# Kernel tuning notes

Hardware: AMD Instinct MI355X
Metric: run time of the kernel (lower is better)

## Reference

```python
import jax, jax.numpy as jnp
import numpy as np

N = 50000      # num vertices
E = 600000     # num incidence pairs
M = 100000     # num hyperedges
IN = 256       # in_channels
H = 8          # heads
C = 32         # out_channels per head


def setup_inputs() -> dict:
    key = jax.random.key(0)
    k = jax.random.split(key, 5)
    X = jax.random.normal(k[0], (N, IN), jnp.float32)
    W = jax.random.normal(k[1], (IN, H * C), jnp.float32) * (1.0 / np.sqrt(IN))
    att_e = jax.random.normal(k[2], (1, H, C), jnp.float32) * 0.1
    vertex = jax.random.randint(k[3], (E,), 0, N)
    edges = jax.random.randint(k[4], (E,), 0, M)
    return {"X": X, "W": W, "att_e": att_e, "vertex": vertex, "edges": edges, "num_edges": M}


def reference(X, W, att_e, vertex, edges, num_edges):
    n, h, c = X.shape[0], att_e.shape[1], att_e.shape[2]
    X0 = X @ W                              # [N, H*C]
    Xh = X0.reshape(n, h, c)                # [N, H, C]
    Xve = Xh[vertex]                        # [E, H, C] gather node feats per incidence
    # mean-aggregate incidences -> hyperedge features
    cnt = jax.ops.segment_sum(jnp.ones((vertex.shape[0],), X.dtype), edges, num_segments=num_edges)
    Xe = jax.ops.segment_sum(Xve, edges, num_segments=num_edges) / jnp.maximum(cnt, 1.0)[:, None, None]  # [M, H, C]
    alpha_e = jnp.sum(Xe * att_e, axis=-1)  # [M, H]
    a_ev = alpha_e[edges]                   # [E, H]
    alpha = jnp.where(a_ev >= 0, a_ev, 0.2 * a_ev)  # leaky_relu(0.2)
    # numerically stable segment softmax over incidences grouped by vertex
    amax = jax.ops.segment_max(alpha, vertex, num_segments=n)[vertex]
    aexp = jnp.exp(alpha - amax)
    asum = jax.ops.segment_sum(aexp, vertex, num_segments=n)[vertex]
    attn = aexp / (asum + 1e-16)            # [E, H]
    Xev = Xe[edges] * attn[:, :, None]      # [E, H, C]
    Xv = jax.ops.segment_sum(Xev, vertex, num_segments=n)  # [N, H, C]
    return jax.nn.gelu(Xv.reshape(n, h * c), approximate=False)
```

## Files before the change

kernel.cpp:

```cpp
#include <hip/hip_runtime.h>
#include <hip/hip_bf16.h>
#include <math.h>

#define NV 50000
#define NE 600000
#define NM 100000
#define KIN 256
#define HCC 256
#define NHH 8

#define NCH 32
#define CHUNK 18750
#define KRANGE 25000
#define HIST_B (NCH * 6)
#define CSCAN_B 74

#define SCAN_NB0 25
#define SCAN_NB1 13

#define CNT_B 2344
#define GEMM_RG 784
#define GEMM_B (GEMM_RG * 4)

typedef unsigned int u32;
typedef unsigned short u16;
typedef _Float16 f16;
typedef _Float16 v8h __attribute__((ext_vector_type(8)));
typedef _Float16 v4h __attribute__((ext_vector_type(4)));
typedef float v4f __attribute__((ext_vector_type(4)));

__global__ __launch_bounds__(256) void k_hist(const int* __restrict__ vertex,
                                              const int* __restrict__ edges,
                                              u16* __restrict__ r_e,
                                              u16* __restrict__ r_v,
                                              u16* __restrict__ Ce,
                                              u16* __restrict__ Cv) {
    __shared__ __align__(16) u32 hist[KRANGE / 2];
    const int bid = blockIdx.x;
    const int t = threadIdx.x;
    const int pass = bid >> 5;
    const int chunk = bid & (NCH - 1);
    const bool eside = pass < 4;
    const int kbase = (eside ? pass : pass - 4) * KRANGE;
    const int* keys = eside ? edges : vertex;
    u16* rout = eside ? r_e : r_v;
    u16* crow = eside ? (Ce + (size_t)chunk * NM) : (Cv + (size_t)chunk * NV);

    uint4* h4 = (uint4*)hist;
    for (int j = t; j < KRANGE / 8; j += 256) h4[j] = make_uint4(0u, 0u, 0u, 0u);
    __syncthreads();

    const int i0 = chunk * CHUNK;
    for (int i = i0 + t; i < i0 + CHUNK; i += 256) {
        int k = keys[i] - kbase;
        if ((u32)k < (u32)KRANGE) {
            int sh = (k & 1) << 4;
            u32 old = atomicAdd(&hist[k >> 1], 1u << sh);
            rout[i] = (u16)(old >> sh);
        }
    }
    __syncthreads();

    uint4* d4 = (uint4*)(crow + kbase);
    for (int j = t; j < KRANGE / 8; j += 256) d4[j] = h4[j];
}

__global__ __launch_bounds__(1024) void k_cscan(u16* __restrict__ Ce,
                                                u16* __restrict__ Cv,
                                                int* __restrict__ e_start,
                                                int* __restrict__ v_start) {
    int tid = blockIdx.x * 1024 + threadIdx.x;
    u32* mat;
    int* outp;
    int col, ncol;
    if (tid < NM / 2)               { mat = (u32*)Ce; outp = e_start; col = tid;          ncol = NM / 2; }
    else if (tid < NM / 2 + NV / 2) { mat = (u32*)Cv; outp = v_start; col = tid - NM / 2; ncol = NV / 2; }
    else return;
    u32 s = 0;
    u32* p = mat + col;
    for (int c = 0; c < NCH; ++c) {
        u32 o = *p;
        *p = s;
        s += o;
        p += ncol;
    }
    outp[2 * col + 1] = (int)(s & 0xffffu);
    outp[2 * col + 2] = (int)(s >> 16);
}

__global__ __launch_bounds__(256) void k_gemm(const float* __restrict__ X,
                                              const float* __restrict__ W,
                                              f16* __restrict__ X0) {
    __shared__ __align__(16) f16 sA[64][72];
    __shared__ __align__(16) f16 sB[64][72];
    const int g = blockIdx.x;
    const int rg = (g >> 5) * 8 + (g & 7);
    const int cg = (g >> 3) & 3;
    if (rg >= (NV + 63) / 64) return;
    const int t = threadIdx.x;
    const int r0 = rg * 64;
    const int c0 = cg * 64;
    const int wave = t >> 6;
    const int lane = t & 63;
    const int quad = lane >> 4;
    const int l16 = lane & 15;
    const int wr = wave & 1;
    const int wc = wave >> 1;

    v4f acc[2][2] = {{{0.f,0.f,0.f,0.f},{0.f,0.f,0.f,0.f}},
                     {{0.f,0.f,0.f,0.f},{0.f,0.f,0.f,0.f}}};

    for (int kc = 0; kc < KIN; kc += 64) {
        __syncthreads();
        #pragma unroll
        for (int i = 0; i < 4; ++i) {
            int lin = i * 256 + t;
            int row = lin >> 4;
            int k = (lin & 15) * 4;
            int gr = r0 + row;
            float4 x = make_float4(0.f, 0.f, 0.f, 0.f);
            if (gr < NV) x = *(const float4*)(X + (size_t)gr * KIN + kc + k);
            v4h hv = { (f16)x.x, (f16)x.y, (f16)x.z, (f16)x.w };
            *(v4h*)&sA[row][k] = hv;
        }
        #pragma unroll
        for (int i = 0; i < 4; ++i) {
            int lin = i * 256 + t;
            int k = lin >> 4;
            int n = (lin & 15) * 4;
            float4 b = *(const float4*)(W + (size_t)(kc + k) * HCC + c0 + n);
            sB[n + 0][k] = (f16)b.x;
            sB[n + 1][k] = (f16)b.y;
            sB[n + 2][k] = (f16)b.z;
            sB[n + 3][k] = (f16)b.w;
        }
        __syncthreads();
        #pragma unroll
        for (int ks = 0; ks < 2; ++ks) {
            const int kb = ks * 32 + quad * 8;
            v8h a[2], b[2];
            #pragma unroll
            for (int rf = 0; rf < 2; ++rf)
                a[rf] = *(const v8h*)&sA[wr * 32 + rf * 16 + l16][kb];
            #pragma unroll
            for (int cf = 0; cf < 2; ++cf)
                b[cf] = *(const v8h*)&sB[wc * 32 + cf * 16 + l16][kb];
            #pragma unroll
            for (int rf = 0; rf < 2; ++rf)
                #pragma unroll
                for (int cf = 0; cf < 2; ++cf)
                    acc[rf][cf] = __builtin_amdgcn_mfma_f32_16x16x32_f16(a[rf], b[cf], acc[rf][cf], 0, 0, 0);
        }
    }
    #pragma unroll
    for (int rf = 0; rf < 2; ++rf)
        #pragma unroll
        for (int cf = 0; cf < 2; ++cf)
            #pragma unroll
            for (int r = 0; r < 4; ++r) {
                int grow = r0 + wr * 32 + rf * 16 + quad * 4 + r;
                if (grow < NV)
                    X0[(size_t)grow * HCC + c0 + wc * 32 + cf * 16 + l16] = (f16)acc[rf][cf][r];
            }
}

__global__ __launch_bounds__(1024) void k_scan_blk(int* __restrict__ a0,
                                                   int* __restrict__ a1,
                                                   int* __restrict__ bsum) {
    const int b = blockIdx.x;
    int* a;
    int n, base;
    if (b < SCAN_NB0) { a = a0; n = NM + 1; base = b * 4096; }
    else              { a = a1; n = NV + 1; base = (b - SCAN_NB0) * 4096; }
    const int t = threadIdx.x;
    const int lane = t & 63, w = t >> 6;
    const int i = base + t * 4;
    int4 v = make_int4(0, 0, 0, 0);
    if (i + 3 < n) v = *(const int4*)(a + i);
    else if (i < n) {
        v.x = a[i];
        if (i + 1 < n) v.y = a[i + 1];
        if (i + 2 < n) v.z = a[i + 2];
    }
    v.y += v.x; v.z += v.y; v.w += v.z;
    int s = v.w;
    #pragma unroll
    for (int d = 1; d < 64; d <<= 1) {
        int x = __shfl_up(s, d, 64);
        if (lane >= d) s += x;
    }
    __shared__ int partials[16];
    __shared__ int woff[16];
    if (lane == 63) partials[w] = s;
    __syncthreads();
    if (t < 16) {
        int p = partials[t];
        int ps = p;
        #pragma unroll
        for (int d = 1; d < 16; d <<= 1) {
            int x = __shfl_up(ps, d, 64);
            if (t >= d) ps += x;
        }
        woff[t] = ps - p;
        if (t == 15) bsum[b] = ps;
    }
    __syncthreads();
    const int add = (s - v.w) + woff[w];
    v.x += add; v.y += add; v.z += add; v.w += add;
    if (i + 3 < n) *(int4*)(a + i) = v;
    else if (i < n) {
        a[i] = v.x;
        if (i + 1 < n) a[i + 1] = v.y;
        if (i + 2 < n) a[i + 2] = v.z;
    }
}

__global__ __launch_bounds__(1024) void k_scan_add(int* __restrict__ a0,
                                                   int* __restrict__ a1,
                                                   const int* __restrict__ bsum) {
    const int b = blockIdx.x;
    int* a;
    int n, bs0, blocal;
    if (b < SCAN_NB0) { a = a0; n = NM + 1; bs0 = 0;        blocal = b; }
    else              { a = a1; n = NV + 1; bs0 = SCAN_NB0; blocal = b - SCAN_NB0; }
    const int t = threadIdx.x;
    const int lane = t & 63;
    int x = (lane < blocal) ? bsum[bs0 + lane] : 0;
    #pragma unroll
    for (int d = 1; d < 64; d <<= 1) x += __shfl_xor(x, d, 64);
    const int off = x;
    const int i = blocal * 4096 + t * 4;
    if (i + 3 < n) {
        int4 v = *(const int4*)(a + i);
        v.x += off; v.y += off; v.z += off; v.w += off;
        *(int4*)(a + i) = v;
    } else if (i < n) {
        a[i] += off;
        if (i + 1 < n) a[i + 1] += off;
        if (i + 2 < n) a[i + 2] += off;
    }
}

__global__ __launch_bounds__(256) void k_efill(const int* __restrict__ vertex,
                                               const int* __restrict__ edges,
                                               const u16* __restrict__ r_e,
                                               const int* __restrict__ e_start,
                                               const u16* __restrict__ Ce,
                                               int* __restrict__ e_list) {
    int i = blockIdx.x * 256 + threadIdx.x;
    if (i >= NE) return;
    int m = edges[i];
    int chunk = i / CHUNK;
    int pos = e_start[m] + (int)Ce[(size_t)chunk * NM + m] + (int)r_e[i];
    e_list[pos] = vertex[i];
}

__global__ __launch_bounds__(256) void k_vfill_egather(const int* __restrict__ vertex,
                                                       const int* __restrict__ edges,
                                                       const u16* __restrict__ r_v,
                                                       const int* __restrict__ v_start,
                                                       const u16* __restrict__ Cv,
                                                       int* __restrict__ v_list,
                                                       const int* __restrict__ e_start,
                                                       const int* __restrict__ e_list,
                                                       const f16* __restrict__ X0,
                                                       const float* __restrict__ att,
                                                       f16* __restrict__ Xe,
                                                       float* __restrict__ alpha_e) {
    const int bid = blockIdx.x;
    if (bid < CNT_B) {
        int i = bid * 256 + threadIdx.x;
        if (i < NE) {
            int v = vertex[i];
            int chunk = i / CHUNK;
            int pos = v_start[v] + (int)Cv[(size_t)chunk * NV + v] + (int)r_v[i];
            v_list[pos] = edges[i];
        }
        return;
    }
    int m = (bid - CNT_B) * 4 + (threadIdx.x >> 6);
    int lane = threadIdx.x & 63;
    int s0 = e_start[m], s1 = e_start[m + 1];
    int c = lane * 4;
    float4 acc = make_float4(0.f, 0.f, 0.f, 0.f);
    int i = s0;
    for (; i + 3 < s1; i += 4) {
        int v0 = e_list[i], v1 = e_list[i + 1], v2 = e_list[i + 2], v3 = e_list[i + 3];
        v4h x0 = *(const v4h*)(X0 + (size_t)v0 * HCC + c);
        v4h x1 = *(const v4h*)(X0 + (size_t)v1 * HCC + c);
        v4h x2 = *(const v4h*)(X0 + (size_t)v2 * HCC + c);
        v4h x3 = *(const v4h*)(X0 + (size_t)v3 * HCC + c);
        acc.x += (float)x0[0] + (float)x1[0] + (float)x2[0] + (float)x3[0];
        acc.y += (float)x0[1] + (float)x1[1] + (float)x2[1] + (float)x3[1];
        acc.z += (float)x0[2] + (float)x1[2] + (float)x2[2] + (float)x3[2];
        acc.w += (float)x0[3] + (float)x1[3] + (float)x2[3] + (float)x3[3];
    }
    for (; i < s1; ++i) {
        int v0 = e_list[i];
        v4h x0 = *(const v4h*)(X0 + (size_t)v0 * HCC + c);
        acc.x += (float)x0[0];
        acc.y += (float)x0[1];
        acc.z += (float)x0[2];
        acc.w += (float)x0[3];
    }
    float inv = 1.0f / fmaxf((float)(s1 - s0), 1.0f);
    acc.x *= inv; acc.y *= inv; acc.z *= inv; acc.w *= inv;
    v4h xev = { (f16)acc.x, (f16)acc.y, (f16)acc.z, (f16)acc.w };
    *(v4h*)(Xe + (size_t)m * HCC + c) = xev;
    float4 av = *(const float4*)(att + c);
    float p = acc.x * av.x + acc.y * av.y + acc.z * av.z + acc.w * av.w;
    p += __shfl_xor(p, 1, 64);
    p += __shfl_xor(p, 2, 64);
    p += __shfl_xor(p, 4, 64);
    if ((lane & 7) == 0) alpha_e[m * NHH + (lane >> 3)] = p;
}

__global__ __launch_bounds__(256) void k_vertex_gather(const int* __restrict__ v_start,
                                                       const int* __restrict__ v_list,
                                                       const f16* __restrict__ Xe,
                                                       const float* __restrict__ alpha_e,
                                                       float* __restrict__ out) {
    int v = blockIdx.x * 4 + (threadIdx.x >> 6);
    int lane = threadIdx.x & 63;
    int s0 = v_start[v], s1 = v_start[v + 1];
    int h = lane >> 3;
    int c = lane * 4;
    float4 acc = make_float4(0.f, 0.f, 0.f, 0.f);
    float se = 0.f;
    int i = s0;
    for (; i + 1 < s1; i += 2) {
        int m0 = v_list[i], m1 = v_list[i + 1];
        float a0 = alpha_e[m0 * NHH + h];
        float a1 = alpha_e[m1 * NHH + h];
        v4h x0 = *(const v4h*)(Xe + (size_t)m0 * HCC + c);
        v4h x1 = *(const v4h*)(Xe + (size_t)m1 * HCC + c);
        a0 = (a0 >= 0.f) ? a0 : 0.2f * a0;
        a1 = (a1 >= 0.f) ? a1 : 0.2f * a1;
        float e0 = __expf(a0);
        float e1 = __expf(a1);
        acc.x += e0 * (float)x0[0] + e1 * (float)x1[0];
        acc.y += e0 * (float)x0[1] + e1 * (float)x1[1];
        acc.z += e0 * (float)x0[2] + e1 * (float)x1[2];
        acc.w += e0 * (float)x0[3] + e1 * (float)x1[3];
        se += e0 + e1;
    }
    if (i < s1) {
        int m0 = v_list[i];
        float a0 = alpha_e[m0 * NHH + h];
        v4h x0 = *(const v4h*)(Xe + (size_t)m0 * HCC + c);
        a0 = (a0 >= 0.f) ? a0 : 0.2f * a0;
        float e0 = __expf(a0);
        acc.x += e0 * (float)x0[0];
        acc.y += e0 * (float)x0[1];
        acc.z += e0 * (float)x0[2];
        acc.w += e0 * (float)x0[3];
        se += e0;
    }
    float inv = 1.0f / (se + 1e-16f);
    float4 o;
    float xx;
    xx = acc.x * inv; o.x = 0.5f * xx * (1.f + erff(xx * 0.70710678118f));
    xx = acc.y * inv; o.y = 0.5f * xx * (1.f + erff(xx * 0.70710678118f));
    xx = acc.z * inv; o.z = 0.5f * xx * (1.f + erff(xx * 0.70710678118f));
    xx = acc.w * inv; o.w = 0.5f * xx * (1.f + erff(xx * 0.70710678118f));
    *(float4*)(out + (size_t)v * HCC + c) = o;
}

extern "C" void kernel_launch(void* const* d_in, const int* in_sizes, int n_in,
                              void* d_out, int out_size, void* d_ws, size_t ws_size,
                              hipStream_t stream) {
    const float* X = (const float*)d_in[0];
    const float* W = (const float*)d_in[1];
    const float* att = (const float*)d_in[2];
    const int* vertex = (const int*)d_in[3];
    const int* edges = (const int*)d_in[4];
    float* out = (float*)d_out;

    char* ws = (char*)d_ws;
    size_t off = 0;
    #define WS_TAKE(bytes) (ws + off); off += (((size_t)(bytes)) + 15) & ~(size_t)15
    f16* X0 = (f16*)WS_TAKE((size_t)NV * HCC * 2);
    f16* Xe = (f16*)WS_TAKE((size_t)NM * HCC * 2);
    float* alpha_e = (float*)WS_TAKE((size_t)NM * NHH * 4);
    size_t z0 = off;
    int* e_start = (int*)WS_TAKE((size_t)(NM + 1) * 4);
    int* v_start = (int*)WS_TAKE((size_t)(NV + 1) * 4);
    size_t z1 = off;
    int* e_list = (int*)WS_TAKE((size_t)NE * 4);
    int* v_list = (int*)WS_TAKE((size_t)NE * 4);
    u16* r_e = (u16*)WS_TAKE((size_t)NE * 2);
    u16* r_v = (u16*)WS_TAKE((size_t)NE * 2);
    u16* Ce = (u16*)WS_TAKE((size_t)NCH * NM * 2);
    u16* Cv = (u16*)WS_TAKE((size_t)NCH * NV * 2);
    int* bsum = (int*)WS_TAKE(64 * 4);
    #undef WS_TAKE

    hipMemsetAsync(e_start, 0, z1 - z0, stream);

    k_hist<<<HIST_B, 256, 0, stream>>>(vertex, edges, r_e, r_v, Ce, Cv);
    k_cscan<<<CSCAN_B, 1024, 0, stream>>>(Ce, Cv, e_start, v_start);
    k_scan_blk<<<SCAN_NB0 + SCAN_NB1, 1024, 0, stream>>>(e_start, v_start, bsum);
    k_scan_add<<<SCAN_NB0 + SCAN_NB1, 1024, 0, stream>>>(e_start, v_start, bsum);
    k_gemm<<<GEMM_B, 256, 0, stream>>>(X, W, X0);
    k_efill<<<CNT_B, 256, 0, stream>>>(vertex, edges, r_e, e_start, Ce, e_list);
    k_vfill_egather<<<CNT_B + NM / 4, 256, 0, stream>>>(vertex, edges, r_v, v_start, Cv, v_list,
                                                        e_start, e_list, X0, att, Xe, alpha_e);
    k_vertex_gather<<<NV / 4, 256, 0, stream>>>(v_start, v_list, Xe, alpha_e, out);
}
```

Baseline: 328.0 us.

## Fuse histogram with GEMM, merge fill kernels, widen gathers to 8-element halves

Histogram and GEMM blocks now run in one launch, with smem shared between the two roles, so the matmul can overlap the counting pass. The histogram chunk count triples to spread the per-key counting over more blocks. The e-list and v-list fills merge into one kernel, and the hyperedge gather becomes its own launch. Both gather kernels now load 8 halves per lane and split incidences across two half-waves, combined with a cross-half shuffle. In exchange, the count matrices and the column scan grow threefold, and every fused-kernel block reserves the large histogram smem, which may limit GEMM occupancy.

Result: no change. 329.5 us (+0.5%).

```diff
diff --git a/kernel.cpp b/kernel.cpp
--- a/kernel.cpp
+++ b/kernel.cpp
@@ -9,10 +9,11 @@
 #define HCC 256
 #define NHH 8
 
-#define NCH 32
-#define CHUNK 18750
+#define NCH 96
+#define CHUNK 6250
 #define KRANGE 25000
-#define HIST_B (NCH * 6)
+#define NPASS 6
+#define HIST_B (NCH * NPASS)
 #define CSCAN_B 74
 
 #define SCAN_NB0 25
@@ -28,41 +29,120 @@
 typedef _Float16 v8h __attribute__((ext_vector_type(8)));
 typedef _Float16 v4h __attribute__((ext_vector_type(4)));
 typedef float v4f __attribute__((ext_vector_type(4)));
-
-__global__ __launch_bounds__(256) void k_hist(const int* __restrict__ vertex,
-                                              const int* __restrict__ edges,
-                                              u16* __restrict__ r_e,
-                                              u16* __restrict__ r_v,
-                                              u16* __restrict__ Ce,
-                                              u16* __restrict__ Cv) {
-    __shared__ __align__(16) u32 hist[KRANGE / 2];
+typedef float v8f __attribute__((ext_vector_type(8)));
+
+__global__ __launch_bounds__(256) void k_hist_gemm(const int* __restrict__ vertex,
+                                                   const int* __restrict__ edges,
+                                                   u16* __restrict__ r_e,
+                                                   u16* __restrict__ r_v,
+                                                   u16* __restrict__ Ce,
+                                                   u16* __restrict__ Cv,
+                                                   const float* __restrict__ X,
+                                                   const float* __restrict__ W,
+                                                   f16* __restrict__ X0) {
+    __shared__ __align__(16) u32 smem[KRANGE / 2];
     const int bid = blockIdx.x;
     const int t = threadIdx.x;
-    const int pass = bid >> 5;
-    const int chunk = bid & (NCH - 1);
-    const bool eside = pass < 4;
-    const int kbase = (eside ? pass : pass - 4) * KRANGE;
-    const int* keys = eside ? edges : vertex;
-    u16* rout = eside ? r_e : r_v;
-    u16* crow = eside ? (Ce + (size_t)chunk * NM) : (Cv + (size_t)chunk * NV);
-
-    uint4* h4 = (uint4*)hist;
-    for (int j = t; j < KRANGE / 8; j += 256) h4[j] = make_uint4(0u, 0u, 0u, 0u);
-    __syncthreads();
-
-    const int i0 = chunk * CHUNK;
-    for (int i = i0 + t; i < i0 + CHUNK; i += 256) {
-        int k = keys[i] - kbase;
-        if ((u32)k < (u32)KRANGE) {
-            int sh = (k & 1) << 4;
-            u32 old = atomicAdd(&hist[k >> 1], 1u << sh);
-            rout[i] = (u16)(old >> sh);
+    if (bid < HIST_B) {
+        u32* hist = smem;
+        const int pass = bid / NCH;
+        const int chunk = bid % NCH;
+        const bool eside = pass < 4;
+        const int kbase = (eside ? pass : pass - 4) * KRANGE;
+        const int* keys = eside ? edges : vertex;
+        u16* rout = eside ? r_e : r_v;
+        u16* crow = eside ? (Ce + (size_t)chunk * NM) : (Cv + (size_t)chunk * NV);
+
+        uint4* h4 = (uint4*)hist;
+        for (int j = t; j < KRANGE / 8; j += 256) h4[j] = make_uint4(0u, 0u, 0u, 0u);
+        __syncthreads();
+
+        const int i0 = chunk * CHUNK;
+        for (int i = i0 + t; i < i0 + CHUNK; i += 256) {
+            int k = keys[i] - kbase;
+            if ((u32)k < (u32)KRANGE) {
+                int sh = (k & 1) << 4;
+                u32 old = atomicAdd(&hist[k >> 1], 1u << sh);
+                rout[i] = (u16)(old >> sh);
+            }
         }
-    }
-    __syncthreads();
-
-    uint4* d4 = (uint4*)(crow + kbase);
-    for (int j = t; j < KRANGE / 8; j += 256) d4[j] = h4[j];
+        __syncthreads();
+
+        uint4* d4 = (uint4*)(crow + kbase);
+        for (int j = t; j < KRANGE / 8; j += 256) d4[j] = h4[j];
+        return;
+    }
+    typedef f16 (*tile_t)[72];
+    tile_t sA = (tile_t)smem;
+    tile_t sB = (tile_t)((char*)smem + 64 * 72 * 2);
+    const int g = bid - HIST_B;
+    const int rg = (g >> 5) * 8 + (g & 7);
+    const int cg = (g >> 3) & 3;
+    if (rg >= (NV + 63) / 64) return;
+    const int r0 = rg * 64;
+    const int c0 = cg * 64;
+    const int wave = t >> 6;
+    const int lane = t & 63;
+    const int quad = lane >> 4;
+    const int l16 = lane & 15;
+    const int wr = wave & 1;
+    const int wc = wave >> 1;
+
+    v4f acc[2][2] = {{{0.f,0.f,0.f,0.f},{0.f,0.f,0.f,0.f}},
+                     {{0.f,0.f,0.f,0.f},{0.f,0.f,0.f,0.f}}};
+
+    for (int kc = 0; kc < KIN; kc += 64) {
+        __syncthreads();
+        #pragma unroll
+        for (int i = 0; i < 4; ++i) {
+            int lin = i * 256 + t;
+            int row = lin >> 4;
+            int k = (lin & 15) * 4;
+            int gr = r0 + row;
+            float4 x = make_float4(0.f, 0.f, 0.f, 0.f);
+            if (gr < NV) x = *(const float4*)(X + (size_t)gr * KIN + kc + k);
+            v4h hv = { (f16)x.x, (f16)x.y, (f16)x.z, (f16)x.w };
+            *(v4h*)&sA[row][k] = hv;
+        }
+        #pragma unroll
+        for (int i = 0; i < 4; ++i) {
+            int lin = i * 256 + t;
+            int k = lin >> 4;
+            int n = (lin & 15) * 4;
+            float4 b = *(const float4*)(W + (size_t)(kc + k) * HCC + c0 + n);
+            sB[n + 0][k] = (f16)b.x;
+            sB[n + 1][k] = (f16)b.y;
+            sB[n + 2][k] = (f16)b.z;
+            sB[n + 3][k] = (f16)b.w;
+        }
+        __syncthreads();
+        #pragma unroll
+        for (int ks = 0; ks < 2; ++ks) {
+            const int kb = ks * 32 + quad * 8;
+            v8h a[2], b[2];
+            #pragma unroll
+            for (int rf = 0; rf < 2; ++rf)
+                a[rf] = *(const v8h*)&sA[wr * 32 + rf * 16 + l16][kb];
+            #pragma unroll
+            for (int cf = 0; cf < 2; ++cf)
+                b[cf] = *(const v8h*)&sB[wc * 32 + cf * 16 + l16][kb];
+            #pragma unroll
+            for (int rf = 0; rf < 2; ++rf)
+                #pragma unroll
+                for (int cf = 0; cf < 2; ++cf)
+                    acc[rf][cf] = __builtin_amdgcn_mfma_f32_16x16x32_f16(a[rf], b[cf], acc[rf][cf], 0, 0, 0);
+        }
+    }
+    #pragma unroll
+    for (int rf = 0; rf < 2; ++rf)
+        #pragma unroll
+        for (int cf = 0; cf < 2; ++cf)
+            #pragma unroll
+            for (int r = 0; r < 4; ++r) {
+                int grow = r0 + wr * 32 + rf * 16 + quad * 4 + r;
+                if (grow < NV)
+                    X0[(size_t)grow * HCC + c0 + wc * 32 + cf * 16 + l16] = (f16)acc[rf][cf][r];
+            }
 }
 
 __global__ __launch_bounds__(1024) void k_cscan(u16* __restrict__ Ce,
@@ -88,82 +168,6 @@
     outp[2 * col + 2] = (int)(s >> 16);
 }
 
-__global__ __launch_bounds__(256) void k_gemm(const float* __restrict__ X,
-                                              const float* __restrict__ W,
-                                              f16* __restrict__ X0) {
-    __shared__ __align__(16) f16 sA[64][72];
-    __shared__ __align__(16) f16 sB[64][72];
-    const int g = blockIdx.x;
-    const int rg = (g >> 5) * 8 + (g & 7);
-    const int cg = (g >> 3) & 3;
-    if (rg >= (NV + 63) / 64) return;
-    const int t = threadIdx.x;
-    const int r0 = rg * 64;
-    const int c0 = cg * 64;
-    const int wave = t >> 6;
-    const int lane = t & 63;
-    const int quad = lane >> 4;
-    const int l16 = lane & 15;
-    const int wr = wave & 1;
-    const int wc = wave >> 1;
-
-    v4f acc[2][2] = {{{0.f,0.f,0.f,0.f},{0.f,0.f,0.f,0.f}},
-                     {{0.f,0.f,0.f,0.f},{0.f,0.f,0.f,0.f}}};
-
-    for (int kc = 0; kc < KIN; kc += 64) {
-        __syncthreads();
-        #pragma unroll
-        for (int i = 0; i < 4; ++i) {
-            int lin = i * 256 + t;
-            int row = lin >> 4;
-            int k = (lin & 15) * 4;
-            int gr = r0 + row;
-            float4 x = make_float4(0.f, 0.f, 0.f, 0.f);
-            if (gr < NV) x = *(const float4*)(X + (size_t)gr * KIN + kc + k);
-            v4h hv = { (f16)x.x, (f16)x.y, (f16)x.z, (f16)x.w };
-            *(v4h*)&sA[row][k] = hv;
-        }
-        #pragma unroll
-        for (int i = 0; i < 4; ++i) {
-            int lin = i * 256 + t;
-            int k = lin >> 4;
-            int n = (lin & 15) * 4;
-            float4 b = *(const float4*)(W + (size_t)(kc + k) * HCC + c0 + n);
-            sB[n + 0][k] = (f16)b.x;
-            sB[n + 1][k] = (f16)b.y;
-            sB[n + 2][k] = (f16)b.z;
-            sB[n + 3][k] = (f16)b.w;
-        }
-        __syncthreads();
-        #pragma unroll
-        for (int ks = 0; ks < 2; ++ks) {
-            const int kb = ks * 32 + quad * 8;
-            v8h a[2], b[2];
-            #pragma unroll
-            for (int rf = 0; rf < 2; ++rf)
-                a[rf] = *(const v8h*)&sA[wr * 32 + rf * 16 + l16][kb];
-            #pragma unroll
-            for (int cf = 0; cf < 2; ++cf)
-                b[cf] = *(const v8h*)&sB[wc * 32 + cf * 16 + l16][kb];
-            #pragma unroll
-            for (int rf = 0; rf < 2; ++rf)
-                #pragma unroll
-                for (int cf = 0; cf < 2; ++cf)
-                    acc[rf][cf] = __builtin_amdgcn_mfma_f32_16x16x32_f16(a[rf], b[cf], acc[rf][cf], 0, 0, 0);
-        }
-    }
-    #pragma unroll
-    for (int rf = 0; rf < 2; ++rf)
-        #pragma unroll
-        for (int cf = 0; cf < 2; ++cf)
-            #pragma unroll
-            for (int r = 0; r < 4; ++r) {
-                int grow = r0 + wr * 32 + rf * 16 + quad * 4 + r;
-                if (grow < NV)
-                    X0[(size_t)grow * HCC + c0 + wc * 32 + cf * 16 + l16] = (f16)acc[rf][cf][r];
-            }
-}
-
 __global__ __launch_bounds__(1024) void k_scan_blk(int* __restrict__ a0,
                                                    int* __restrict__ a1,
                                                    int* __restrict__ bsum) {
@@ -241,129 +245,129 @@
     }
 }
 
-__global__ __launch_bounds__(256) void k_efill(const int* __restrict__ vertex,
+__global__ __launch_bounds__(256) void k_fill2(const int* __restrict__ vertex,
                                                const int* __restrict__ edges,
                                                const u16* __restrict__ r_e,
+                                               const u16* __restrict__ r_v,
                                                const int* __restrict__ e_start,
+                                               const int* __restrict__ v_start,
                                                const u16* __restrict__ Ce,
-                                               int* __restrict__ e_list) {
+                                               const u16* __restrict__ Cv,
+                                               int* __restrict__ e_list,
+                                               int* __restrict__ v_list) {
     int i = blockIdx.x * 256 + threadIdx.x;
     if (i >= NE) return;
-    int m = edges[i];
+    int v = vertex[i], m = edges[i];
     int chunk = i / CHUNK;
-    int pos = e_start[m] + (int)Ce[(size_t)chunk * NM + m] + (int)r_e[i];
-    e_list[pos] = vertex[i];
-}
-
-__global__ __launch_bounds__(256) void k_vfill_egather(const int* __restrict__ vertex,
-                                                       const int* __restrict__ edges,
-                                                       const u16* __restrict__ r_v,
-                                                       const int* __restrict__ v_start,
-                                                       const u16* __restrict__ Cv,
-                                                       int* __restrict__ v_list,
-                                                       const int* __restrict__ e_start,
-                                                       const int* __restrict__ e_list,
-                                                       const f16* __restrict__ X0,
-                                                       const float* __restrict__ att,
-                                                       f16* __restrict__ Xe,
-                                                       float* __restrict__ alpha_e) {
-    const int bid = blockIdx.x;
-    if (bid < CNT_B) {
-        int i = bid * 256 + threadIdx.x;
-        if (i < NE) {
-            int v = vertex[i];
-            int chunk = i / CHUNK;
-            int pos = v_start[v] + (int)Cv[(size_t)chunk * NV + v] + (int)r_v[i];
-            v_list[pos] = edges[i];
-        }
-        return;
-    }
-    int m = (bid - CNT_B) * 4 + (threadIdx.x >> 6);
+    int pe = e_start[m] + (int)Ce[(size_t)chunk * NM + m] + (int)r_e[i];
+    e_list[pe] = v;
+    int pv = v_start[v] + (int)Cv[(size_t)chunk * NV + v] + (int)r_v[i];
+    v_list[pv] = m;
+}
+
+__global__ __launch_bounds__(256) void k_egather(const int* __restrict__ e_start,
+                                                 const int* __restrict__ e_list,
+                                                 const f16* __restrict__ X0,
+                                                 const float* __restrict__ att,
+                                                 f16* __restrict__ Xe,
+                                                 float* __restrict__ alpha_e) {
+    int m = blockIdx.x * 4 + (threadIdx.x >> 6);
     int lane = threadIdx.x & 63;
+    int half = lane >> 5;
+    int l32 = lane & 31;
+    int c8 = l32 * 8;
     int s0 = e_start[m], s1 = e_start[m + 1];
-    int c = lane * 4;
-    float4 acc = make_float4(0.f, 0.f, 0.f, 0.f);
-    int i = s0;
-    for (; i + 3 < s1; i += 4) {
-        int v0 = e_list[i], v1 = e_list[i + 1], v2 = e_list[i + 2], v3 = e_list[i + 3];
-        v4h x0 = *(const v4h*)(X0 + (size_t)v0 * HCC + c);
-        v4h x1 = *(const v4h*)(X0 + (size_t)v1 * HCC + c);
-        v4h x2 = *(const v4h*)(X0 + (size_t)v2 * HCC + c);
-        v4h x3 = *(const v4h*)(X0 + (size_t)v3 * HCC + c);
-        acc.x += (float)x0[0] + (float)x1[0] + (float)x2[0] + (float)x3[0];
-        acc.y += (float)x0[1] + (float)x1[1] + (float)x2[1] + (float)x3[1];
-        acc.z += (float)x0[2] + (float)x1[2] + (float)x2[2] + (float)x3[2];
-        acc.w += (float)x0[3] + (float)x1[3] + (float)x2[3] + (float)x3[3];
-    }
-    for (; i < s1; ++i) {
+    v8f acc = {0.f,0.f,0.f,0.f,0.f,0.f,0.f,0.f};
+    int i = s0 + half;
+    for (; i + 2 < s1; i += 4) {
+        int v0 = e_list[i], v1 = e_list[i + 2];
+        v8h x0 = *(const v8h*)(X0 + (size_t)v0 * HCC + c8);
+        v8h x1 = *(const v8h*)(X0 + (size_t)v1 * HCC + c8);
+        #pragma unroll
+        for (int j = 0; j < 8; ++j) acc[j] += (float)x0[j] + (float)x1[j];
+    }
+    if (i < s1) {
         int v0 = e_list[i];
-        v4h x0 = *(const v4h*)(X0 + (size_t)v0 * HCC + c);
-        acc.x += (float)x0[0];
-        acc.y += (float)x0[1];
-        acc.z += (float)x0[2];
-        acc.w += (float)x0[3];
-    }
+        v8h x0 = *(const v8h*)(X0 + (size_t)v0 * HCC + c8);
+        #pragma unroll
+        for (int j = 0; j < 8; ++j) acc[j] += (float)x0[j];
+    }
+    #pragma unroll
+    for (int j = 0; j < 8; ++j) acc[j] += __shfl_xor(acc[j], 32, 64);
     float inv = 1.0f / fmaxf((float)(s1 - s0), 1.0f);
-    acc.x *= inv; acc.y *= inv; acc.z *= inv; acc.w *= inv;
-    v4h xev = { (f16)acc.x, (f16)acc.y, (f16)acc.z, (f16)acc.w };
-    *(v4h*)(Xe + (size_t)m * HCC + c) = xev;
-    float4 av = *(const float4*)(att + c);
-    float p = acc.x * av.x + acc.y * av.y + acc.z * av.z + acc.w * av.w;
+    #pragma unroll
+    for (int j = 0; j < 8; ++j) acc[j] *= inv;
+    if (half == 0) {
+        v8h xv;
+        #pragma unroll
+        for (int j = 0; j < 8; ++j) xv[j] = (f16)acc[j];
+        *(v8h*)(Xe + (size_t)m * HCC + c8) = xv;
+    }
+    float4 a0 = *(const float4*)(att + c8);
+    float4 a1 = *(const float4*)(att + c8 + 4);
+    float p = acc[0]*a0.x + acc[1]*a0.y + acc[2]*a0.z + acc[3]*a0.w
+            + acc[4]*a1.x + acc[5]*a1.y + acc[6]*a1.z + acc[7]*a1.w;
     p += __shfl_xor(p, 1, 64);
     p += __shfl_xor(p, 2, 64);
-    p += __shfl_xor(p, 4, 64);
-    if ((lane & 7) == 0) alpha_e[m * NHH + (lane >> 3)] = p;
-}
-
-__global__ __launch_bounds__(256) void k_vertex_gather(const int* __restrict__ v_start,
-                                                       const int* __restrict__ v_list,
-                                                       const f16* __restrict__ Xe,
-                                                       const float* __restrict__ alpha_e,
-                                                       float* __restrict__ out) {
+    if (half == 0 && (l32 & 3) == 0) alpha_e[m * NHH + (l32 >> 2)] = p;
+}
+
+__global__ __launch_bounds__(256) void k_vgather(const int* __restrict__ v_start,
+                                                 const int* __restrict__ v_list,
+                                                 const f16* __restrict__ Xe,
+                                                 const float* __restrict__ alpha_e,
+                                                 float* __restrict__ out) {
     int v = blockIdx.x * 4 + (threadIdx.x >> 6);
     int lane = threadIdx.x & 63;
+    int half = lane >> 5;
+    int l32 = lane & 31;
+    int h = l32 >> 2;
+    int c8 = l32 * 8;
     int s0 = v_start[v], s1 = v_start[v + 1];
-    int h = lane >> 3;
-    int c = lane * 4;
-    float4 acc = make_float4(0.f, 0.f, 0.f, 0.f);
+    v8f acc = {0.f,0.f,0.f,0.f,0.f,0.f,0.f,0.f};
     float se = 0.f;
-    int i = s0;
-    for (; i + 1 < s1; i += 2) {
-        int m0 = v_list[i], m1 = v_list[i + 1];
+    int i = s0 + half;
+    for (; i + 2 < s1; i += 4) {
+        int m0 = v_list[i], m1 = v_list[i + 2];
         float a0 = alpha_e[m0 * NHH + h];
         float a1 = alpha_e[m1 * NHH + h];
-        v4h x0 = *(const v4h*)(Xe + (size_t)m0 * HCC + c);
-        v4h x1 = *(const v4h*)(Xe + (size_t)m1 * HCC + c);
+        v8h x0 = *(const v8h*)(Xe + (size_t)m0 * HCC + c8);
+        v8h x1 = *(const v8h*)(Xe + (size_t)m1 * HCC + c8);
         a0 = (a0 >= 0.f) ? a0 : 0.2f * a0;
         a1 = (a1 >= 0.f) ? a1 : 0.2f * a1;
         float e0 = __expf(a0);
         float e1 = __expf(a1);
-        acc.x += e0 * (float)x0[0] + e1 * (float)x1[0];
-        acc.y += e0 * (float)x0[1] + e1 * (float)x1[1];
-        acc.z += e0 * (float)x0[2] + e1 * (float)x1[2];
-        acc.w += e0 * (float)x0[3] + e1 * (float)x1[3];
+        #pragma unroll
+        for (int j = 0; j < 8; ++j) acc[j] += e0 * (float)x0[j] + e1 * (float)x1[j];
         se += e0 + e1;
     }
     if (i < s1) {
         int m0 = v_list[i];
         float a0 = alpha_e[m0 * NHH + h];
-        v4h x0 = *(const v4h*)(Xe + (size_t)m0 * HCC + c);
+        v8h x0 = *(const v8h*)(Xe + (size_t)m0 * HCC + c8);
         a0 = (a0 >= 0.f) ? a0 : 0.2f * a0;
         float e0 = __expf(a0);
-        acc.x += e0 * (float)x0[0];
-        acc.y += e0 * (float)x0[1];
-        acc.z += e0 * (float)x0[2];
-        acc.w += e0 * (float)x0[3];
+        #pragma unroll
+        for (int j = 0; j < 8; ++j) acc[j] += e0 * (float)x0[j];
         se += e0;
     }
+    #pragma unroll
+    for (int j = 0; j < 8; ++j) acc[j] += __shfl_xor(acc[j], 32, 64);
+    se += __shfl_xor(se, 32, 64);
+    if (half) return;
     float inv = 1.0f / (se + 1e-16f);
-    float4 o;
+    float4 o0, o1;
     float xx;
-    xx = acc.x * inv; o.x = 0.5f * xx * (1.f + erff(xx * 0.70710678118f));
-    xx = acc.y * inv; o.y = 0.5f * xx * (1.f + erff(xx * 0.70710678118f));
-    xx = acc.z * inv; o.z = 0.5f * xx * (1.f + erff(xx * 0.70710678118f));
-    xx = acc.w * inv; o.w = 0.5f * xx * (1.f + erff(xx * 0.70710678118f));
-    *(float4*)(out + (size_t)v * HCC + c) = o;
+    xx = acc[0] * inv; o0.x = 0.5f * xx * (1.f + erff(xx * 0.70710678118f));
+    xx = acc[1] * inv; o0.y = 0.5f * xx * (1.f + erff(xx * 0.70710678118f));
+    xx = acc[2] * inv; o0.z = 0.5f * xx * (1.f + erff(xx * 0.70710678118f));
+    xx = acc[3] * inv; o0.w = 0.5f * xx * (1.f + erff(xx * 0.70710678118f));
+    xx = acc[4] * inv; o1.x = 0.5f * xx * (1.f + erff(xx * 0.70710678118f));
+    xx = acc[5] * inv; o1.y = 0.5f * xx * (1.f + erff(xx * 0.70710678118f));
+    xx = acc[6] * inv; o1.z = 0.5f * xx * (1.f + erff(xx * 0.70710678118f));
+    xx = acc[7] * inv; o1.w = 0.5f * xx * (1.f + erff(xx * 0.70710678118f));
+    *(float4*)(out + (size_t)v * HCC + c8) = o0;
+    *(float4*)(out + (size_t)v * HCC + c8 + 4) = o1;
 }
 
 extern "C" void kernel_launch(void* const* d_in, const int* in_sizes, int n_in,
@@ -397,13 +401,13 @@
 
     hipMemsetAsync(e_start, 0, z1 - z0, stream);
 
-    k_hist<<<HIST_B, 256, 0, stream>>>(vertex, edges, r_e, r_v, Ce, Cv);
+    k_hist_gemm<<<HIST_B + GEMM_B, 256, 0, stream>>>(vertex, edges, r_e, r_v, Ce, Cv,
+                                                     X, W, X0);
     k_cscan<<<CSCAN_B, 1024, 0, stream>>>(Ce, Cv, e_start, v_start);
     k_scan_blk<<<SCAN_NB0 + SCAN_NB1, 1024, 0, stream>>>(e_start, v_start, bsum);
     k_scan_add<<<SCAN_NB0 + SCAN_NB1, 1024, 0, stream>>>(e_start, v_start, bsum);
-    k_gemm<<<GEMM_B, 256, 0, stream>>>(X, W, X0);
-    k_efill<<<CNT_B, 256, 0, stream>>>(vertex, edges, r_e, e_start, Ce, e_list);
-    k_vfill_egather<<<CNT_B + NM / 4, 256, 0, stream>>>(vertex, edges, r_v, v_start, Cv, v_list,
-                                                        e_start, e_list, X0, att, Xe, alpha_e);
-    k_vertex_gather<<<NV / 4, 256, 0, stream>>>(v_start, v_list, Xe, alpha_e, out);
-}
+    k_fill2<<<CNT_B, 256, 0, stream>>>(vertex, edges, r_e, r_v, e_start, v_start,
+                                       Ce, Cv, e_list, v_list);
+    k_egather<<<NM / 4, 256, 0, stream>>>(e_start, e_list, X0, att, Xe, alpha_e);
+    k_vgather<<<NV / 4, 256, 0, stream>>>(v_start, v_list, Xe, alpha_e, out);
+}
```
